# Kernel tuning notes

Hardware: AMD Instinct MI355X
Metric: run time of the kernel (lower is better)

The kernel has to match this reference:

```python
import jax, jax.numpy as jnp
import numpy as np


def conv3x3(x, w, b):
    # x: [B,1,H,W], w: [1,1,3,3] (OIHW), b: [1]; stride 1, padding 1
    y = jax.lax.conv_general_dilated(x, w, (1, 1), 'SAME',
                                     dimension_numbers=('NCHW', 'OIHW', 'NCHW'))
    return y + b[0]


def avg_pool(x, k):
    B, C, H, W = x.shape
    return x.reshape(B, C, H // k, k, W // k, k).mean(axis=(3, 5))


def nearest_up(x, k):
    # nearest-neighbor upsample by integer factor k (matches torch 'nearest')
    return jnp.repeat(jnp.repeat(x, k, axis=2), k, axis=3)


def conv1x1(x, w):
    # x: [B,3,H,W], w: [1,3,1,1] -> [B,1,H,W]
    return jnp.einsum('bchw,oc->bohw', x, w[:, :, 0, 0])


def setup_inputs() -> dict:
    key = jax.random.key(0)
    ks = jax.random.split(key, 16)
    B, H, W = 8, 512, 512
    std = 0.005
    inp = {
        'x':          jax.random.normal(ks[0], (B, 1, H, W), jnp.float32),
        'downSample': jax.random.normal(ks[1], (B, 1, H // 2, W // 2), jnp.float32),
        'upSample':   jax.random.normal(ks[2], (B, 1, 2 * H, 2 * W), jnp.float32),
        'BU':         jax.random.normal(ks[3], (B, 1, H, W), jnp.float32),
        'BUdown':     jax.random.normal(ks[4], (B, 1, H // 2, W // 2), jnp.float32),
        'BUup':       jax.random.normal(ks[5], (B, 1, 2 * H, 2 * W), jnp.float32),
        'convAx': std * jax.random.normal(ks[6], (1, 1, 3, 3), jnp.float32),
        'biasx':  std * jax.random.normal(ks[7], (1,), jnp.float32),
        'convAd': std * jax.random.normal(ks[8], (1, 1, 3, 3), jnp.float32),
        'biasd':  std * jax.random.normal(ks[9], (1,), jnp.float32),
        'convAu': std * jax.random.normal(ks[10], (1, 1, 3, 3), jnp.float32),
        'biasu':  std * jax.random.normal(ks[11], (1,), jnp.float32),
        'conv1x1_x': std * jax.random.normal(ks[12], (1, 3, 1, 1), jnp.float32),
        'conv1x1_d': std * jax.random.normal(ks[13], (1, 3, 1, 1), jnp.float32),
        'conv1x1_u': std * jax.random.normal(ks[14], (1, 3, 1, 1), jnp.float32),
    }
    return inp


def reference(x, downSample, upSample, BU, BUdown, BUup,
              convAx, biasx, convAd, biasd, convAu, biasu,
              conv1x1_x, conv1x1_d, conv1x1_u):
    # 5 iterations of conv3x3 + residual add + clamp(-1,1) per pyramid level
    for _ in range(5):
        x = jnp.clip(conv3x3(x, convAx, biasx) + BU, -1.0, 1.0)
        downSample = jnp.clip(conv3x3(downSample, convAd, biasd) + BUdown, -1.0, 1.0)
        upSample = jnp.clip(conv3x3(upSample, convAu, biasu) + BUup, -1.0, 1.0)
    # cross-scale fusion: resample all three levels to each level and concat
    newx = jnp.concatenate([avg_pool(upSample, 2), x, nearest_up(downSample, 2)], axis=1)
    newUp = jnp.concatenate([upSample, nearest_up(x, 2), nearest_up(downSample, 4)], axis=1)
    newDown = jnp.concatenate([avg_pool(upSample, 4), avg_pool(x, 2), downSample], axis=1)
    x_out = conv1x1(newx, conv1x1_x)
    down_out = conv1x1(newDown, conv1x1_d)
    up_out = conv1x1(newUp, conv1x1_u)
    return (x_out, down_out, up_out)
```

## Files before the change

### kernel.cpp

```cpp
#include <hip/hip_runtime.h>

#define NBATCH 8
#define TW 64
#define TH 32
#define SROWS 42
#define SQUADS 20
#define STRDQ 96
#define NSTRIP 180
#define NTHR 192

__device__ __forceinline__ int lofs(int R, int q) {
    int p = q + (3 * (R >> 1)) % 24;
    if (p >= 24) p -= 24;
    return R * STRDQ + (p << 2);
}

__device__ __forceinline__ void acc_row(float4& v, float L, float4 m, float R,
                                        float ka, float kb, float kc) {
    v.x += ka * L   + kb * m.x + kc * m.y;
    v.y += ka * m.x + kb * m.y + kc * m.z;
    v.z += ka * m.y + kb * m.z + kc * m.w;
    v.w += ka * m.z + kb * m.w + kc * R;
}

__global__ __launch_bounds__(NTHR, 4) void conv5_all(
    const float* __restrict__ srcU, const float* __restrict__ buU,
    const float* __restrict__ wtU, const float* __restrict__ bsU,
    const float* __restrict__ srcX, const float* __restrict__ buX,
    const float* __restrict__ wtX, const float* __restrict__ bsX,
    const float* __restrict__ srcD, const float* __restrict__ buD,
    const float* __restrict__ wtD, const float* __restrict__ bsD,
    float* __restrict__ dstU, float* __restrict__ dstX, float* __restrict__ dstD)
{
    __shared__ __align__(16) float bufA[SROWS * STRDQ];
    __shared__ __align__(16) float bufB[SROWS * STRDQ];

    const int tid = threadIdx.x;
    const int blk = blockIdx.x;

    const float* src; const float* BU; const float* wt; const float* bs;
    float* dst; int HW; int tx, ty, b;
    if (blk < 4096) {
        src = srcU; BU = buU; wt = wtU; bs = bsU; dst = dstU; HW = 1024;
        b = blk >> 9; int rem = blk & 511; ty = rem >> 4; tx = rem & 15;
    } else if (blk < 5120) {
        int t = blk - 4096;
        src = srcX; BU = buX; wt = wtX; bs = bsX; dst = dstX; HW = 512;
        b = t >> 7; int rem = t & 127; ty = rem >> 3; tx = rem & 7;
    } else {
        int t = blk - 5120;
        src = srcD; BU = buD; wt = wtD; bs = bsD; dst = dstD; HW = 256;
        b = t >> 5; int rem = t & 31; ty = rem >> 2; tx = rem & 3;
    }
    const int bh0 = ty * TH, bw0 = tx * TW;
    const long base = (long)b * HW * HW;

    for (int s = tid; s < SROWS * SQUADS; s += NTHR) {
        int r = s / SQUADS, cq = s - r * SQUADS;
        int gh = bh0 + r - 5;
        int gw = bw0 + (cq << 2) - 8;
        float4 v = {0.0f, 0.0f, 0.0f, 0.0f};
        if ((unsigned)gh < (unsigned)HW) {
            const float* gp = src + base + (long)gh * HW + gw;
            if (gw >= 0 && gw + 3 < HW) {
                v = *(const float4*)gp;
            } else {
                if ((unsigned)(gw + 0) < (unsigned)HW) v.x = gp[0];
                if ((unsigned)(gw + 1) < (unsigned)HW) v.y = gp[1];
                if ((unsigned)(gw + 2) < (unsigned)HW) v.z = gp[2];
                if ((unsigned)(gw + 3) < (unsigned)HW) v.w = gp[3];
            }
        }
        *(float4*)&bufA[lofs(r, cq)] = v;
    }

    const float k00 = wt[0], k01 = wt[1], k02 = wt[2];
    const float k10 = wt[3], k11 = wt[4], k12 = wt[5];
    const float k20 = wt[6], k21 = wt[7], k22 = wt[8];
    const float bias = bs[0];

    const bool act = (tid < NSTRIP);
    int sc = act ? tid : 0;
    int rp = sc / 9, j = sc - rp * 9;

    int rdo[4][4];
    #pragma unroll
    for (int r = 0; r < 4; ++r)
        #pragma unroll
        for (int c = 0; c < 4; ++c)
            rdo[r][c] = lofs(2 * rp + r, 2 * j + c);
    int wro[2][2];
    #pragma unroll
    for (int i = 0; i < 2; ++i) {
        wro[i][0] = lofs(2 * rp + 1 + i, 2 * j + 1);
        wro[i][1] = lofs(2 * rp + 1 + i, 2 * j + 2);
    }

    float4 wf0, wf1;
    {
        float* p0 = (float*)&wf0; float* p1 = (float*)&wf1;
        #pragma unroll
        for (int k = 0; k < 4; ++k) {
            p0[k] = ((unsigned)(bw0 + 8 * j - 4 + k) < (unsigned)HW) ? 1.0f : 0.0f;
            p1[k] = ((unsigned)(bw0 + 8 * j + k)     < (unsigned)HW) ? 1.0f : 0.0f;
        }
    }
    float hf[2];
    float4 bu0[2], bu1[2];
    #pragma unroll
    for (int i = 0; i < 2; ++i) {
        int gh = bh0 + 2 * rp - 4 + i;
        bool hok = act && ((unsigned)gh < (unsigned)HW);
        hf[i] = hok ? 1.0f : 0.0f;
        int gw0 = bw0 + 8 * j - 4;
        const float* bp = BU + base + (long)gh * HW + gw0;
        if (hok && gw0 >= 0 && gw0 + 7 < HW) {
            float4 a = *(const float4*)bp;
            float4 c = *(const float4*)(bp + 4);
            bu0[i] = {a.x + bias, a.y + bias, a.z + bias, a.w + bias};
            bu1[i] = {c.x + bias, c.y + bias, c.z + bias, c.w + bias};
        } else {
            float* b0 = (float*)&bu0[i]; float* b1 = (float*)&bu1[i];
            #pragma unroll
            for (int k = 0; k < 4; ++k) {
                int w0 = gw0 + k;
                int w1 = gw0 + 4 + k;
                b0[k] = (hok && (unsigned)w0 < (unsigned)HW) ? (bp[k] + bias)     : 0.0f;
                b1[k] = (hok && (unsigned)w1 < (unsigned)HW) ? (bp[k + 4] + bias) : 0.0f;
            }
        }
    }

    float* cur = bufA;
    float* nxt = bufB;

    for (int it = 0; it < 5; ++it) {
        __syncthreads();
        if (act) {
            float4 q[4][4];
            #pragma unroll
            for (int r = 0; r < 4; ++r)
                #pragma unroll
                for (int c = 0; c < 4; ++c)
                    q[r][c] = *(const float4*)(cur + rdo[r][c]);
            #pragma unroll
            for (int i = 0; i < 2; ++i) {
                float4 v0 = bu0[i];
                float4 v1 = bu1[i];
                acc_row(v0, q[i][0].w,     q[i][1],     q[i][2].x,     k00, k01, k02);
                acc_row(v0, q[i + 1][0].w, q[i + 1][1], q[i + 1][2].x, k10, k11, k12);
                acc_row(v0, q[i + 2][0].w, q[i + 2][1], q[i + 2][2].x, k20, k21, k22);
                acc_row(v1, q[i][1].w,     q[i][2],     q[i][3].x,     k00, k01, k02);
                acc_row(v1, q[i + 1][1].w, q[i + 1][2], q[i + 1][3].x, k10, k11, k12);
                acc_row(v1, q[i + 2][1].w, q[i + 2][2], q[i + 2][3].x, k20, k21, k22);
                float m = hf[i];
                v0.x = fminf(1.0f, fmaxf(-1.0f, v0.x)) * (m * wf0.x);
                v0.y = fminf(1.0f, fmaxf(-1.0f, v0.y)) * (m * wf0.y);
                v0.z = fminf(1.0f, fmaxf(-1.0f, v0.z)) * (m * wf0.z);
                v0.w = fminf(1.0f, fmaxf(-1.0f, v0.w)) * (m * wf0.w);
                v1.x = fminf(1.0f, fmaxf(-1.0f, v1.x)) * (m * wf1.x);
                v1.y = fminf(1.0f, fmaxf(-1.0f, v1.y)) * (m * wf1.y);
                v1.z = fminf(1.0f, fmaxf(-1.0f, v1.z)) * (m * wf1.z);
                v1.w = fminf(1.0f, fmaxf(-1.0f, v1.w)) * (m * wf1.w);
                *(float4*)(nxt + wro[i][0]) = v0;
                *(float4*)(nxt + wro[i][1]) = v1;
            }
        }
        float* t = cur; cur = nxt; nxt = t;
    }
    __syncthreads();

    for (int i2 = tid; i2 < TH * (TW / 4); i2 += NTHR) {
        int r = i2 >> 4;
        int cq = i2 & 15;
        float4 v = *(const float4*)&cur[lofs(r + 5, cq + 2)];
        *(float4*)&dst[base + (long)(bh0 + r) * HW + bw0 + (cq << 2)] = v;
    }
}

__global__ __launch_bounds__(256) void fuse_all(
    const float* __restrict__ X,
    const float* __restrict__ D,
    const float* __restrict__ U,
    const float* __restrict__ cx,
    const float* __restrict__ cd,
    const float* __restrict__ cu,
    float* __restrict__ xo, float* __restrict__ dno, float* __restrict__ upo)
{
    const int total = NBATCH << 16;
    int idx = blockIdx.x * blockDim.x + threadIdx.x;
    if (idx >= total) return;
    int wd = idx & 255;
    int hd = (idx >> 8) & 255;
    int b  = idx >> 16;

    const float cx0 = cx[0], cx1 = cx[1], cx2 = cx[2];
    const float cd0 = cd[0], cd1 = cd[1], cd2 = cd[2];
    const float cu0 = cu[0], cu1 = cu[1], cu2 = cu[2];

    int ub = (b << 20) + ((hd << 2) << 10) + (wd << 2);
    float4 u0 = *(const float4*)&U[ub];
    float4 u1 = *(const float4*)&U[ub + 1024];
    float4 u2 = *(const float4*)&U[ub + 2048];
    float4 u3 = *(const float4*)&U[ub + 3072];
    int xb = (b << 18) + ((hd << 1) << 9) + (wd << 1);
    float2 x0 = *(const float2*)&X[xb];
    float2 x1 = *(const float2*)&X[xb + 512];
    float dv = D[idx];

    float p00 = 0.25f * (u0.x + u0.y + u1.x + u1.y);
    float p01 = 0.25f * (u0.z + u0.w + u1.z + u1.w);
    float p10 = 0.25f * (u2.x + u2.y + u3.x + u3.y);
    float p11 = 0.25f * (u2.z + u2.w + u3.z + u3.w);
    float pu4 = 0.25f * (p00 + p01 + p10 + p11);
    float px2 = 0.25f * (x0.x + x0.y + x1.x + x1.y);

    dno[idx] = cd0 * pu4 + cd1 * px2 + cd2 * dv;

    float2 xo0, xo1;
    xo0.x = cx0 * p00 + cx1 * x0.x + cx2 * dv;
    xo0.y = cx0 * p01 + cx1 * x0.y + cx2 * dv;
    xo1.x = cx0 * p10 + cx1 * x1.x + cx2 * dv;
    xo1.y = cx0 * p11 + cx1 * x1.y + cx2 * dv;
    *(float2*)&xo[xb]       = xo0;
    *(float2*)&xo[xb + 512] = xo1;

    float4 o0, o1, o2, o3;
    o0.x = cu0 * u0.x + cu1 * x0.x + cu2 * dv;
    o0.y = cu0 * u0.y + cu1 * x0.x + cu2 * dv;
    o0.z = cu0 * u0.z + cu1 * x0.y + cu2 * dv;
    o0.w = cu0 * u0.w + cu1 * x0.y + cu2 * dv;
    o1.x = cu0 * u1.x + cu1 * x0.x + cu2 * dv;
    o1.y = cu0 * u1.y + cu1 * x0.x + cu2 * dv;
    o1.z = cu0 * u1.z + cu1 * x0.y + cu2 * dv;
    o1.w = cu0 * u1.w + cu1 * x0.y + cu2 * dv;
    o2.x = cu0 * u2.x + cu1 * x1.x + cu2 * dv;
    o2.y = cu0 * u2.y + cu1 * x1.x + cu2 * dv;
    o2.z = cu0 * u2.z + cu1 * x1.y + cu2 * dv;
    o2.w = cu0 * u2.w + cu1 * x1.y + cu2 * dv;
    o3.x = cu0 * u3.x + cu1 * x1.x + cu2 * dv;
    o3.y = cu0 * u3.y + cu1 * x1.x + cu2 * dv;
    o3.z = cu0 * u3.z + cu1 * x1.y + cu2 * dv;
    o3.w = cu0 * u3.w + cu1 * x1.y + cu2 * dv;
    *(float4*)&upo[ub]        = o0;
    *(float4*)&upo[ub + 1024] = o1;
    *(float4*)&upo[ub + 2048] = o2;
    *(float4*)&upo[ub + 3072] = o3;
}

extern "C" void kernel_launch(void* const* d_in, const int* in_sizes, int n_in,
                              void* d_out, int out_size, void* d_ws, size_t ws_size,
                              hipStream_t stream)
{
    const float* x    = (const float*)d_in[0];
    const float* down = (const float*)d_in[1];
    const float* up   = (const float*)d_in[2];
    const float* BUx  = (const float*)d_in[3];
    const float* BUd  = (const float*)d_in[4];
    const float* BUu  = (const float*)d_in[5];
    const float* wAx  = (const float*)d_in[6];
    const float* bx   = (const float*)d_in[7];
    const float* wAd  = (const float*)d_in[8];
    const float* bd   = (const float*)d_in[9];
    const float* wAu  = (const float*)d_in[10];
    const float* bu   = (const float*)d_in[11];
    const float* c1x  = (const float*)d_in[12];
    const float* c1d  = (const float*)d_in[13];
    const float* c1u  = (const float*)d_in[14];

    float* out = (float*)d_out;
    float* ws  = (float*)d_ws;

    const int NX = NBATCH * 512 * 512;
    const int ND = NBATCH * 256 * 256;

    float* wsX = ws;
    float* wsD = ws + NX;
    float* wsU = ws + NX + ND;
    float* outX = out;
    float* outD = out + NX;
    float* outU = out + NX + ND;

    conv5_all<<<5376, NTHR, 0, stream>>>(
        up,   BUu, wAu, bu,
        x,    BUx, wAx, bx,
        down, BUd, wAd, bd,
        wsU, wsX, wsD);

    fuse_all<<<(ND + 255) / 256, 256, 0, stream>>>(wsX, wsD, wsU, c1x, c1d, c1u,
                                                   outX, outD, outU);
}
```

Before: 217.8 us.

## Shrink LDS row stride, remap thread-to-strip assignment, fuse clamp via fmed3

New measurement: 208.4 us. 4.3% less time.

```diff
diff --git a/kernel.cpp b/kernel.cpp
--- a/kernel.cpp
+++ b/kernel.cpp
@@ -5,13 +5,14 @@
 #define TH 32
 #define SROWS 42
 #define SQUADS 20
-#define STRDQ 96
+#define STRDQ 80
 #define NSTRIP 180
 #define NTHR 192
 
 __device__ __forceinline__ int lofs(int R, int q) {
-    int p = q + (3 * (R >> 1)) % 24;
-    if (p >= 24) p -= 24;
+    int rot = (3 * (R >> 1)) % 20;
+    int p = q + rot;
+    if (p >= 20) p -= 20;
     return R * STRDQ + (p << 2);
 }
 
@@ -21,6 +22,13 @@
     v.y += ka * m.x + kb * m.y + kc * m.z;
     v.z += ka * m.y + kb * m.z + kc * m.w;
     v.w += ka * m.z + kb * m.w + kc * R;
+}
+
+__device__ __forceinline__ void clamp_mask(float4& v, float4 pm) {
+    v.x = __builtin_amdgcn_fmed3f(v.x, -1.0f, 1.0f) * pm.x;
+    v.y = __builtin_amdgcn_fmed3f(v.y, -1.0f, 1.0f) * pm.y;
+    v.z = __builtin_amdgcn_fmed3f(v.z, -1.0f, 1.0f) * pm.z;
+    v.w = __builtin_amdgcn_fmed3f(v.w, -1.0f, 1.0f) * pm.w;
 }
 
 __global__ __launch_bounds__(NTHR, 4) void conv5_all(
@@ -73,6 +81,13 @@
         }
         *(float4*)&bufA[lofs(r, cq)] = v;
     }
+    for (int s = tid; s < 120; s += NTHR) {
+        int r, q;
+        if (s < 40)      { r = (s < 20) ? 0 : 41; q = s % 20; }
+        else             { int s2 = s - 40; r = 1 + (s2 >> 1); q = (s2 & 1) ? 19 : 0; }
+        float4 z = {0.0f, 0.0f, 0.0f, 0.0f};
+        *(float4*)&bufB[lofs(r, q)] = z;
+    }
 
     const float k00 = wt[0], k01 = wt[1], k02 = wt[2];
     const float k10 = wt[3], k11 = wt[4], k12 = wt[5];
@@ -80,8 +95,17 @@
     const float bias = bs[0];
 
     const bool act = (tid < NSTRIP);
-    int sc = act ? tid : 0;
-    int rp = sc / 9, j = sc - rp * 9;
+    int rp = 0, j = 0;
+    {
+        int g = (0x75426310u >> ((tid & 7) << 2)) & 0xF;
+        int need = tid >> 3;
+        for (int r_ = (g & 1); r_ < 20; r_ += 2) {
+            int j0 = ((g - 3 * r_) & 7) >> 1;
+            int c = (j0 == 0) ? 3 : 2;
+            if (need < c) { rp = r_; j = j0 + 4 * need; break; }
+            need -= c;
+        }
+    }
 
     int rdo[4][4];
     #pragma unroll
@@ -96,22 +120,24 @@
         wro[i][1] = lofs(2 * rp + 1 + i, 2 * j + 2);
     }
 
-    float4 wf0, wf1;
-    {
-        float* p0 = (float*)&wf0; float* p1 = (float*)&wf1;
+    float4 pm0[2], pm1[2];
+    float hf[2];
+    #pragma unroll
+    for (int i = 0; i < 2; ++i) {
+        int gh = bh0 + 2 * rp - 4 + i;
+        hf[i] = (act && (unsigned)gh < (unsigned)HW) ? 1.0f : 0.0f;
+        float* p0 = (float*)&pm0[i]; float* p1 = (float*)&pm1[i];
         #pragma unroll
         for (int k = 0; k < 4; ++k) {
-            p0[k] = ((unsigned)(bw0 + 8 * j - 4 + k) < (unsigned)HW) ? 1.0f : 0.0f;
-            p1[k] = ((unsigned)(bw0 + 8 * j + k)     < (unsigned)HW) ? 1.0f : 0.0f;
-        }
-    }
-    float hf[2];
+            p0[k] = hf[i] * (((unsigned)(bw0 + 8 * j - 4 + k) < (unsigned)HW) ? 1.0f : 0.0f);
+            p1[k] = hf[i] * (((unsigned)(bw0 + 8 * j + k)     < (unsigned)HW) ? 1.0f : 0.0f);
+        }
+    }
     float4 bu0[2], bu1[2];
     #pragma unroll
     for (int i = 0; i < 2; ++i) {
         int gh = bh0 + 2 * rp - 4 + i;
-        bool hok = act && ((unsigned)gh < (unsigned)HW);
-        hf[i] = hok ? 1.0f : 0.0f;
+        bool hok = (hf[i] != 0.0f);
         int gw0 = bw0 + 8 * j - 4;
         const float* bp = BU + base + (long)gh * HW + gw0;
         if (hok && gw0 >= 0 && gw0 + 7 < HW) {
@@ -153,15 +179,8 @@
                 acc_row(v1, q[i][1].w,     q[i][2],     q[i][3].x,     k00, k01, k02);
                 acc_row(v1, q[i + 1][1].w, q[i + 1][2], q[i + 1][3].x, k10, k11, k12);
                 acc_row(v1, q[i + 2][1].w, q[i + 2][2], q[i + 2][3].x, k20, k21, k22);
-                float m = hf[i];
-                v0.x = fminf(1.0f, fmaxf(-1.0f, v0.x)) * (m * wf0.x);
-                v0.y = fminf(1.0f, fmaxf(-1.0f, v0.y)) * (m * wf0.y);
-                v0.z = fminf(1.0f, fmaxf(-1.0f, v0.z)) * (m * wf0.z);
-                v0.w = fminf(1.0f, fmaxf(-1.0f, v0.w)) * (m * wf0.w);
-                v1.x = fminf(1.0f, fmaxf(-1.0f, v1.x)) * (m * wf1.x);
-                v1.y = fminf(1.0f, fmaxf(-1.0f, v1.y)) * (m * wf1.y);
-                v1.z = fminf(1.0f, fmaxf(-1.0f, v1.z)) * (m * wf1.z);
-                v1.w = fminf(1.0f, fmaxf(-1.0f, v1.w)) * (m * wf1.w);
+                clamp_mask(v0, pm0[i]);
+                clamp_mask(v1, pm1[i]);
                 *(float4*)(nxt + wro[i][0]) = v0;
                 *(float4*)(nxt + wro[i][1]) = v1;
             }
```
